# Kernel tuning notes

Hardware: AMD Instinct MI355X
Metric: run time of the kernel (lower is better)

The kernel has to match this reference:

```python
import jax, jax.numpy as jnp
import numpy as np


def setup_inputs() -> dict:
    key = jax.random.key(0)
    k1, k2, k3 = jax.random.split(key, 3)
    b, c, h, w = 4, 64, 64, 64
    content = jax.random.normal(k1, (b, c, h, w), dtype=jnp.float32)
    content_s = jax.random.normal(k2, (b, c, h, w), dtype=jnp.float32)
    style = jax.random.normal(k3, (b, c, h, w), dtype=jnp.float32)
    return {"content": content, "content_s": content_s, "style": style}


def reference(content, content_s, style):
    b, c, h, w = content.shape
    hw = h * w
    Fc = content.reshape(b, c, hw)      # [b, c, HW]
    Fs = content_s.reshape(b, c, hw)    # [b, c, HW]
    Fst = style.reshape(b, c, hw)       # [b, c, HW]
    # S[b, q, k] = sum_c Fc[b, c, q] * Fs[b, c, k]  (Fc transposed as in torch)
    S = jnp.einsum('bcq,bck->bqk', Fc, Fs)
    S = jax.nn.softmax(S, axis=-1)
    # O = style @ S^T : O[b, c, q] = sum_k Fst[b, c, k] * S[b, q, k]
    O = jnp.einsum('bck,bqk->bcq', Fst, S).reshape(b, c, h, w)
    return jnp.concatenate((content, O), axis=1)
```

## Files before the change

kernel.cpp:

```cpp
#include <hip/hip_runtime.h>
#include <math.h>


#define Bb 4
#define Cc 64
#define HWs 4096
#define SPLITS 4
#define TILES_PER_SPLIT 16
#define RLOG2E 1.44269504088896340736f

typedef _Float16 half8 __attribute__((ext_vector_type(8)));
typedef _Float16 half4 __attribute__((ext_vector_type(4)));
typedef float floatx4 __attribute__((ext_vector_type(4)));

__global__ __launch_bounds__(256) void prep_k(const float* __restrict__ content,
                                              const float* __restrict__ Fs,
                                              const float* __restrict__ Fst,
                                              float* __restrict__ out,
                                              _Float16* __restrict__ Kt,
                                              _Float16* __restrict__ Vt) {
    const int bid = blockIdx.x;
    const int t = threadIdx.x;
    if (bid < 1024) {
        int i4 = bid * 256 + t;
        const float4* c4 = (const float4*)content;
        const float4* v4 = (const float4*)Fst;
        float4* o4 = (float4*)out;
        int b = i4 >> 16, rem = i4 & 65535;
        o4[(size_t)b * 131072 + rem] = c4[i4];
        float4 v = v4[i4];
        half4 h;
        h[0] = (_Float16)v.x; h[1] = (_Float16)v.y;
        h[2] = (_Float16)v.z; h[3] = (_Float16)v.w;
        *(half4*)(Vt + (size_t)i4 * 4) = h;
    } else {
        __shared__ _Float16 T[16][72];
        int e = bid - 1024;
        int b = e >> 8;
        int hw0 = (e & 255) * 16;
        const float* sb = Fs + (size_t)b * Cc * HWs;
        {
            int c = t >> 2, x4 = (t & 3) * 4;
            float4 v = *(const float4*)(sb + (size_t)c * HWs + hw0 + x4);
            T[x4 + 0][c] = (_Float16)v.x;
            T[x4 + 1][c] = (_Float16)v.y;
            T[x4 + 2][c] = (_Float16)v.z;
            T[x4 + 3][c] = (_Float16)v.w;
        }
        __syncthreads();
        if (t < 128) {
            int row = t >> 3, g = t & 7;
            _Float16* db = Kt + (size_t)b * HWs * Cc;
            *(half8*)(db + (size_t)(hw0 + row) * Cc + g * 8) = *(half8*)&T[row][g * 8];
        }
    }
}

__global__ __launch_bounds__(512, 4) void attn_k(const float* __restrict__ Fc,
                                                 const _Float16* __restrict__ Kt,
                                                 const _Float16* __restrict__ Vt,
                                                 float* __restrict__ Opart,
                                                 float2* __restrict__ ml) {
    const int tid  = threadIdx.x;
    const int w    = tid >> 6;
    const int lane = tid & 63;
    const int quad = lane >> 4;
    const int l15  = lane & 15;
    const int qg = blockIdx.x & 31;
    const int b  = (blockIdx.x >> 5) & 3;
    const int s  = blockIdx.x >> 7;
    const int k0base = s * TILES_PER_SPLIT * 64;
    const int q = qg * 128 + w * 16 + l15;

    __shared__ _Float16 Kl[2][64 * 64];
    __shared__ _Float16 Vl[2][64 * 64];
    __shared__ _Float16 Ps[8][16][80];

    const float*    Fcb = Fc + (size_t)b * Cc * HWs;
    const _Float16* Kb  = Kt + (size_t)b * HWs * Cc;
    const _Float16* Vb  = Vt + (size_t)b * Cc * HWs;

    const bool isK  = tid < 256;
    const int  sl   = tid & 255;
    const int  srow = sl >> 3;
    const int  sjg  = sl & 7;
    const int  ssw  = (sjg ^ (srow & 7)) * 8;

    half8 qf0, qf1;
    #pragma unroll
    for (int j = 0; j < 8; ++j) {
        qf0[j] = (_Float16)(Fcb[(size_t)(quad * 8 + j) * HWs + q] * RLOG2E);
        qf1[j] = (_Float16)(Fcb[(size_t)(32 + quad * 8 + j) * HWs + q] * RLOG2E);
    }

    half8 st0, st1;
    auto stage_load = [&](int kt) {
        int kk0 = k0base + kt * 64;
        if (isK) {
            st0 = *(const half8*)(Kb + (size_t)(kk0 + srow) * 64 + sjg * 8);
            st1 = *(const half8*)(Kb + (size_t)(kk0 + 32 + srow) * 64 + sjg * 8);
        } else {
            st0 = *(const half8*)(Vb + (size_t)srow * HWs + kk0 + sjg * 8);
            st1 = *(const half8*)(Vb + (size_t)(32 + srow) * HWs + kk0 + sjg * 8);
        }
    };
    auto stage_write = [&](int p) {
        if (isK) {
            *(half8*)&Kl[p][srow * 64 + ssw]        = st0;
            *(half8*)&Kl[p][(32 + srow) * 64 + ssw] = st1;
        } else {
            *(half8*)&Vl[p][srow * 64 + ssw]        = st0;
            *(half8*)&Vl[p][(32 + srow) * 64 + ssw] = st1;
        }
    };

    floatx4 acc[4];
    #pragma unroll
    for (int m = 0; m < 4; ++m) acc[m] = (floatx4)(0.0f);
    float m_run = -INFINITY, lsum = 0.0f;

    stage_load(0);
    stage_write(0);
    stage_load(1);
    __syncthreads();

    const int swl = (l15 & 7);
    for (int kt = 0; kt < TILES_PER_SPLIT; ++kt) {
        const int p = kt & 1;
        if (kt + 1 < TILES_PER_SPLIT) stage_write(p ^ 1);
        if (kt + 2 < TILES_PER_SPLIT) stage_load(kt + 2);

        half8 ka[4][2];
        #pragma unroll
        for (int m = 0; m < 4; ++m)
            #pragma unroll
            for (int cs = 0; cs < 2; ++cs)
                ka[m][cs] = *(const half8*)&Kl[p][(m * 16 + l15) * 64 + (((cs * 4 + quad) ^ swl) * 8)];

        floatx4 sv[4];
        #pragma unroll
        for (int m = 0; m < 4; ++m) {
            sv[m] = __builtin_amdgcn_mfma_f32_16x16x32_f16(ka[m][0], qf0, (floatx4)(0.0f), 0, 0, 0);
            sv[m] = __builtin_amdgcn_mfma_f32_16x16x32_f16(ka[m][1], qf1, sv[m], 0, 0, 0);
        }

        half8 va[4][2];
        #pragma unroll
        for (int m = 0; m < 4; ++m)
            #pragma unroll
            for (int ks = 0; ks < 2; ++ks)
                va[m][ks] = *(const half8*)&Vl[p][(m * 16 + l15) * 64 + (((ks * 4 + quad) ^ swl) * 8)];

        float mx = -INFINITY;
        #pragma unroll
        for (int m = 0; m < 4; ++m)
            #pragma unroll
            for (int r = 0; r < 4; ++r) mx = fmaxf(mx, sv[m][r]);
        mx = fmaxf(mx, __shfl_xor(mx, 16));
        mx = fmaxf(mx, __shfl_xor(mx, 32));
        float m_new = fmaxf(m_run, mx);
        float alpha = exp2f(m_run - m_new);
        m_run = m_new;
        float part = 0.0f;
        #pragma unroll
        for (int m = 0; m < 4; ++m)
            #pragma unroll
            for (int r = 0; r < 4; ++r) {
                float e = exp2f(sv[m][r] - m_new);
                sv[m][r] = e;
                part += e;
            }
        lsum = lsum * alpha + part;
        #pragma unroll
        for (int m = 0; m < 4; ++m)
            #pragma unroll
            for (int r = 0; r < 4; ++r) acc[m][r] *= alpha;

        #pragma unroll
        for (int m = 0; m < 4; ++m) {
            half4 pp;
            pp[0] = (_Float16)sv[m][0]; pp[1] = (_Float16)sv[m][1];
            pp[2] = (_Float16)sv[m][2]; pp[3] = (_Float16)sv[m][3];
            *(half4*)&Ps[w][l15][m * 16 + quad * 4] = pp;
        }
        half8 pb0 = *(half8*)&Ps[w][l15][quad * 8];
        half8 pb1 = *(half8*)&Ps[w][l15][32 + quad * 8];

        #pragma unroll
        for (int m = 0; m < 4; ++m) {
            acc[m] = __builtin_amdgcn_mfma_f32_16x16x32_f16(va[m][0], pb0, acc[m], 0, 0, 0);
            acc[m] = __builtin_amdgcn_mfma_f32_16x16x32_f16(va[m][1], pb1, acc[m], 0, 0, 0);
        }

        __syncthreads();
    }

    lsum += __shfl_xor(lsum, 16);
    lsum += __shfl_xor(lsum, 32);

    float* op = Opart + (((size_t)s * Bb + b) * Cc) * HWs;
    #pragma unroll
    for (int m = 0; m < 4; ++m)
        #pragma unroll
        for (int r = 0; r < 4; ++r) {
            int c = m * 16 + quad * 4 + r;
            op[(size_t)c * HWs + q] = acc[m][r];
        }
    if (quad == 0)
        ml[((size_t)b * HWs + q) * SPLITS + s] = make_float2(m_run, lsum);
}

__global__ __launch_bounds__(256) void combine_k(const float* __restrict__ Opart,
                                                 const float2* __restrict__ ml,
                                                 float* __restrict__ out) {
    int idx = blockIdx.x * 256 + threadIdx.x;
    int q = idx & 4095;
    int c = (idx >> 12) & 63;
    int b = idx >> 18;
    const float2* mlp = ml + ((size_t)b * HWs + q) * SPLITS;
    float2 mls[SPLITS];
    #pragma unroll
    for (int s = 0; s < SPLITS; ++s) mls[s] = mlp[s];
    float M = -INFINITY;
    #pragma unroll
    for (int s = 0; s < SPLITS; ++s) M = fmaxf(M, mls[s].x);
    float l = 0.0f, wgt[SPLITS];
    #pragma unroll
    for (int s = 0; s < SPLITS; ++s) {
        wgt[s] = exp2f(mls[s].x - M);
        l += wgt[s] * mls[s].y;
    }
    float o = 0.0f;
    #pragma unroll
    for (int s = 0; s < SPLITS; ++s)
        o += wgt[s] * Opart[(((size_t)s * Bb + b) * Cc + c) * HWs + q];
    out[((size_t)b * 2 * Cc + Cc + c) * HWs + q] = o / l;
}

extern "C" void kernel_launch(void* const* d_in, const int* in_sizes, int n_in,
                              void* d_out, int out_size, void* d_ws, size_t ws_size,
                              hipStream_t stream) {
    const float* content   = (const float*)d_in[0];
    const float* content_s = (const float*)d_in[1];
    const float* style     = (const float*)d_in[2];
    float* out = (float*)d_out;

    _Float16* Kt = (_Float16*)d_ws;
    _Float16* Vt = Kt + (size_t)Bb * HWs * Cc;
    float*    Opart = (float*)(Vt + (size_t)Bb * Cc * HWs);
    float2*   ml = (float2*)(Opart + (size_t)SPLITS * Bb * Cc * HWs);

    prep_k<<<dim3(2048), dim3(256), 0, stream>>>(content, content_s, style, out, Kt, Vt);
    attn_k<<<dim3(SPLITS * Bb * 32), dim3(512), 0, stream>>>(content, Kt, Vt, Opart, ml);
    combine_k<<<dim3(4096), dim3(256), 0, stream>>>(Opart, ml, out);
}
```

Measured before the change: 111.1 us.

## Process two query groups per wave and store split partials in fp16

Each wave now handles 32 queries as two 16-query groups. K and V fragments loaded from LDS are reused across both groups, and the block shrinks to 256 threads covering the same 128 queries. The split-K partial outputs are written and read as fp16 instead of fp32, halving that intermediate traffic between attention and combine. In exchange, register pressure and per-wave serial work rise, occupancy drops, and the fp16 partials lose precision.

```diff
diff --git a/kernel.cpp b/kernel.cpp
--- a/kernel.cpp
+++ b/kernel.cpp
@@ -56,10 +56,10 @@
     }
 }
 
-__global__ __launch_bounds__(512, 4) void attn_k(const float* __restrict__ Fc,
+__global__ __launch_bounds__(256, 2) void attn_k(const float* __restrict__ Fc,
                                                  const _Float16* __restrict__ Kt,
                                                  const _Float16* __restrict__ Vt,
-                                                 float* __restrict__ Opart,
+                                                 _Float16* __restrict__ Opart,
                                                  float2* __restrict__ ml) {
     const int tid  = threadIdx.x;
     const int w    = tid >> 6;
@@ -70,54 +70,58 @@
     const int b  = (blockIdx.x >> 5) & 3;
     const int s  = blockIdx.x >> 7;
     const int k0base = s * TILES_PER_SPLIT * 64;
-    const int q = qg * 128 + w * 16 + l15;
+    const int qA = qg * 128 + w * 32 + l15;
+    const int qB = qA + 16;
 
     __shared__ _Float16 Kl[2][64 * 64];
     __shared__ _Float16 Vl[2][64 * 64];
-    __shared__ _Float16 Ps[8][16][80];
+    __shared__ _Float16 Ps[4][32][72];
 
     const float*    Fcb = Fc + (size_t)b * Cc * HWs;
     const _Float16* Kb  = Kt + (size_t)b * HWs * Cc;
     const _Float16* Vb  = Vt + (size_t)b * Cc * HWs;
 
-    const bool isK  = tid < 256;
-    const int  sl   = tid & 255;
+    const bool isK  = tid < 128;
+    const int  sl   = tid & 127;
     const int  srow = sl >> 3;
     const int  sjg  = sl & 7;
     const int  ssw  = (sjg ^ (srow & 7)) * 8;
 
-    half8 qf0, qf1;
+    half8 qf[2][2];
     #pragma unroll
     for (int j = 0; j < 8; ++j) {
-        qf0[j] = (_Float16)(Fcb[(size_t)(quad * 8 + j) * HWs + q] * RLOG2E);
-        qf1[j] = (_Float16)(Fcb[(size_t)(32 + quad * 8 + j) * HWs + q] * RLOG2E);
-    }
-
-    half8 st0, st1;
+        qf[0][0][j] = (_Float16)(Fcb[(size_t)(quad * 8 + j) * HWs + qA] * RLOG2E);
+        qf[0][1][j] = (_Float16)(Fcb[(size_t)(32 + quad * 8 + j) * HWs + qA] * RLOG2E);
+        qf[1][0][j] = (_Float16)(Fcb[(size_t)(quad * 8 + j) * HWs + qB] * RLOG2E);
+        qf[1][1][j] = (_Float16)(Fcb[(size_t)(32 + quad * 8 + j) * HWs + qB] * RLOG2E);
+    }
+
+    half8 st[4];
     auto stage_load = [&](int kt) {
         int kk0 = k0base + kt * 64;
-        if (isK) {
-            st0 = *(const half8*)(Kb + (size_t)(kk0 + srow) * 64 + sjg * 8);
-            st1 = *(const half8*)(Kb + (size_t)(kk0 + 32 + srow) * 64 + sjg * 8);
-        } else {
-            st0 = *(const half8*)(Vb + (size_t)srow * HWs + kk0 + sjg * 8);
-            st1 = *(const half8*)(Vb + (size_t)(32 + srow) * HWs + kk0 + sjg * 8);
+        #pragma unroll
+        for (int i = 0; i < 4; ++i) {
+            int row = srow + 16 * i;
+            if (isK) st[i] = *(const half8*)(Kb + (size_t)(kk0 + row) * 64 + sjg * 8);
+            else     st[i] = *(const half8*)(Vb + (size_t)row * HWs + kk0 + sjg * 8);
         }
     };
     auto stage_write = [&](int p) {
-        if (isK) {
-            *(half8*)&Kl[p][srow * 64 + ssw]        = st0;
-            *(half8*)&Kl[p][(32 + srow) * 64 + ssw] = st1;
-        } else {
-            *(half8*)&Vl[p][srow * 64 + ssw]        = st0;
-            *(half8*)&Vl[p][(32 + srow) * 64 + ssw] = st1;
+        #pragma unroll
+        for (int i = 0; i < 4; ++i) {
+            int row = srow + 16 * i;
+            if (isK) *(half8*)&Kl[p][row * 64 + ssw] = st[i];
+            else     *(half8*)&Vl[p][row * 64 + ssw] = st[i];
         }
     };
 
-    floatx4 acc[4];
-    #pragma unroll
-    for (int m = 0; m < 4; ++m) acc[m] = (floatx4)(0.0f);
-    float m_run = -INFINITY, lsum = 0.0f;
+    floatx4 acc[2][4];
+    #pragma unroll
+    for (int g = 0; g < 2; ++g)
+        #pragma unroll
+        for (int m = 0; m < 4; ++m) acc[g][m] = (floatx4)(0.0f);
+    float m_run[2] = {-INFINITY, -INFINITY};
+    float lsum[2] = {0.0f, 0.0f};
 
     stage_load(0);
     stage_write(0);
@@ -137,11 +141,14 @@
             for (int cs = 0; cs < 2; ++cs)
                 ka[m][cs] = *(const half8*)&Kl[p][(m * 16 + l15) * 64 + (((cs * 4 + quad) ^ swl) * 8)];
 
-        floatx4 sv[4];
+        floatx4 sv[2][4];
         #pragma unroll
         for (int m = 0; m < 4; ++m) {
-            sv[m] = __builtin_amdgcn_mfma_f32_16x16x32_f16(ka[m][0], qf0, (floatx4)(0.0f), 0, 0, 0);
-            sv[m] = __builtin_amdgcn_mfma_f32_16x16x32_f16(ka[m][1], qf1, sv[m], 0, 0, 0);
+            #pragma unroll
+            for (int g = 0; g < 2; ++g) {
+                sv[g][m] = __builtin_amdgcn_mfma_f32_16x16x32_f16(ka[m][0], qf[g][0], (floatx4)(0.0f), 0, 0, 0);
+                sv[g][m] = __builtin_amdgcn_mfma_f32_16x16x32_f16(ka[m][1], qf[g][1], sv[g][m], 0, 0, 0);
+            }
         }
 
         half8 va[4][2];
@@ -151,66 +158,75 @@
             for (int ks = 0; ks < 2; ++ks)
                 va[m][ks] = *(const half8*)&Vl[p][(m * 16 + l15) * 64 + (((ks * 4 + quad) ^ swl) * 8)];
 
-        float mx = -INFINITY;
-        #pragma unroll
-        for (int m = 0; m < 4; ++m)
-            #pragma unroll
-            for (int r = 0; r < 4; ++r) mx = fmaxf(mx, sv[m][r]);
-        mx = fmaxf(mx, __shfl_xor(mx, 16));
-        mx = fmaxf(mx, __shfl_xor(mx, 32));
-        float m_new = fmaxf(m_run, mx);
-        float alpha = exp2f(m_run - m_new);
-        m_run = m_new;
-        float part = 0.0f;
+        half8 pb[2][2];
+        #pragma unroll
+        for (int g = 0; g < 2; ++g) {
+            float mx = -INFINITY;
+            #pragma unroll
+            for (int m = 0; m < 4; ++m)
+                #pragma unroll
+                for (int r = 0; r < 4; ++r) mx = fmaxf(mx, sv[g][m][r]);
+            mx = fmaxf(mx, __shfl_xor(mx, 16));
+            mx = fmaxf(mx, __shfl_xor(mx, 32));
+            float m_new = fmaxf(m_run[g], mx);
+            float alpha = exp2f(m_run[g] - m_new);
+            m_run[g] = m_new;
+            float part = 0.0f;
+            #pragma unroll
+            for (int m = 0; m < 4; ++m)
+                #pragma unroll
+                for (int r = 0; r < 4; ++r) {
+                    float e = exp2f(sv[g][m][r] - m_new);
+                    sv[g][m][r] = e;
+                    part += e;
+                }
+            lsum[g] = lsum[g] * alpha + part;
+            #pragma unroll
+            for (int m = 0; m < 4; ++m)
+                #pragma unroll
+                for (int r = 0; r < 4; ++r) acc[g][m][r] *= alpha;
+
+            #pragma unroll
+            for (int m = 0; m < 4; ++m) {
+                half4 pp;
+                pp[0] = (_Float16)sv[g][m][0]; pp[1] = (_Float16)sv[g][m][1];
+                pp[2] = (_Float16)sv[g][m][2]; pp[3] = (_Float16)sv[g][m][3];
+                *(half4*)&Ps[w][g * 16 + l15][m * 16 + quad * 4] = pp;
+            }
+            pb[g][0] = *(half8*)&Ps[w][g * 16 + l15][quad * 8];
+            pb[g][1] = *(half8*)&Ps[w][g * 16 + l15][32 + quad * 8];
+        }
+
+        #pragma unroll
+        for (int m = 0; m < 4; ++m)
+            #pragma unroll
+            for (int g = 0; g < 2; ++g) {
+                acc[g][m] = __builtin_amdgcn_mfma_f32_16x16x32_f16(va[m][0], pb[g][0], acc[g][m], 0, 0, 0);
+                acc[g][m] = __builtin_amdgcn_mfma_f32_16x16x32_f16(va[m][1], pb[g][1], acc[g][m], 0, 0, 0);
+            }
+
+        __syncthreads();
+    }
+
+    _Float16* op = Opart + (((size_t)s * Bb + b) * Cc) * HWs;
+    #pragma unroll
+    for (int g = 0; g < 2; ++g) {
+        lsum[g] += __shfl_xor(lsum[g], 16);
+        lsum[g] += __shfl_xor(lsum[g], 32);
+        int q = (g == 0) ? qA : qB;
         #pragma unroll
         for (int m = 0; m < 4; ++m)
             #pragma unroll
             for (int r = 0; r < 4; ++r) {
-                float e = exp2f(sv[m][r] - m_new);
-                sv[m][r] = e;
-                part += e;
-            }
-        lsum = lsum * alpha + part;
-        #pragma unroll
-        for (int m = 0; m < 4; ++m)
-            #pragma unroll
-            for (int r = 0; r < 4; ++r) acc[m][r] *= alpha;
-
-        #pragma unroll
-        for (int m = 0; m < 4; ++m) {
-            half4 pp;
-            pp[0] = (_Float16)sv[m][0]; pp[1] = (_Float16)sv[m][1];
-            pp[2] = (_Float16)sv[m][2]; pp[3] = (_Float16)sv[m][3];
-            *(half4*)&Ps[w][l15][m * 16 + quad * 4] = pp;
-        }
-        half8 pb0 = *(half8*)&Ps[w][l15][quad * 8];
-        half8 pb1 = *(half8*)&Ps[w][l15][32 + quad * 8];
-
-        #pragma unroll
-        for (int m = 0; m < 4; ++m) {
-            acc[m] = __builtin_amdgcn_mfma_f32_16x16x32_f16(va[m][0], pb0, acc[m], 0, 0, 0);
-            acc[m] = __builtin_amdgcn_mfma_f32_16x16x32_f16(va[m][1], pb1, acc[m], 0, 0, 0);
-        }
-
-        __syncthreads();
-    }
-
-    lsum += __shfl_xor(lsum, 16);
-    lsum += __shfl_xor(lsum, 32);
-
-    float* op = Opart + (((size_t)s * Bb + b) * Cc) * HWs;
-    #pragma unroll
-    for (int m = 0; m < 4; ++m)
-        #pragma unroll
-        for (int r = 0; r < 4; ++r) {
-            int c = m * 16 + quad * 4 + r;
-            op[(size_t)c * HWs + q] = acc[m][r];
-        }
-    if (quad == 0)
-        ml[((size_t)b * HWs + q) * SPLITS + s] = make_float2(m_run, lsum);
-}
-
-__global__ __launch_bounds__(256) void combine_k(const float* __restrict__ Opart,
+                int c = m * 16 + quad * 4 + r;
+                op[(size_t)c * HWs + q] = (_Float16)acc[g][m][r];
+            }
+        if (quad == 0)
+            ml[((size_t)b * HWs + q) * SPLITS + s] = make_float2(m_run[g], lsum[g]);
+    }
+}
+
+__global__ __launch_bounds__(256) void combine_k(const _Float16* __restrict__ Opart,
                                                  const float2* __restrict__ ml,
                                                  float* __restrict__ out) {
     int idx = blockIdx.x * 256 + threadIdx.x;
@@ -233,7 +249,7 @@
     float o = 0.0f;
     #pragma unroll
     for (int s = 0; s < SPLITS; ++s)
-        o += wgt[s] * Opart[(((size_t)s * Bb + b) * Cc + c) * HWs + q];
+        o += wgt[s] * (float)Opart[(((size_t)s * Bb + b) * Cc + c) * HWs + q];
     out[((size_t)b * 2 * Cc + Cc + c) * HWs + q] = o / l;
 }
 
@@ -247,10 +263,10 @@
 
     _Float16* Kt = (_Float16*)d_ws;
     _Float16* Vt = Kt + (size_t)Bb * HWs * Cc;
-    float*    Opart = (float*)(Vt + (size_t)Bb * Cc * HWs);
+    _Float16* Opart = Vt + (size_t)Bb * Cc * HWs;
     float2*   ml = (float2*)(Opart + (size_t)SPLITS * Bb * Cc * HWs);
 
     prep_k<<<dim3(2048), dim3(256), 0, stream>>>(content, content_s, style, out, Kt, Vt);
-    attn_k<<<dim3(SPLITS * Bb * 32), dim3(512), 0, stream>>>(content, Kt, Vt, Opart, ml);
+    attn_k<<<dim3(SPLITS * Bb * 32), dim3(256), 0, stream>>>(content, Kt, Vt, Opart, ml);
     combine_k<<<dim3(4096), dim3(256), 0, stream>>>(Opart, ml, out);
 }
```

New measurement: 110.1 us. About the same (-0.9%).
